# Kernel optimization log

Hardware: AMD Instinct MI355X
Metric: run time of the kernel (lower is better)

The kernel has to match this reference:

```python
import jax, jax.numpy as jnp
import numpy as np

N_NODES = 50000
N_EDGES = 1600000
IN_SIZE = 128
HIDDEN = 128
OUT_SIZE = 64
NUM_LAYERS = 3
BN_EPS = 1e-5
GIN_EPS_INIT = 1e-5


def setup_inputs() -> dict:
    key = jax.random.key(0)
    ks = jax.random.split(key, 16)
    node_feat = jax.random.normal(ks[0], (N_NODES, IN_SIZE), dtype=jnp.float32)
    src = jax.random.randint(ks[1], (N_EDGES,), 0, N_NODES)
    dst = jax.random.randint(ks[2], (N_EDGES,), 0, N_NODES)
    # per-layer MLP params (in_size == hidden, so shapes are uniform across layers)
    s1 = 1.0 / np.sqrt(IN_SIZE)
    s2 = 1.0 / np.sqrt(HIDDEN)
    W1 = jax.random.uniform(ks[3], (NUM_LAYERS, IN_SIZE, HIDDEN), jnp.float32, -s1, s1)
    b1 = jax.random.uniform(ks[4], (NUM_LAYERS, HIDDEN), jnp.float32, -s1, s1)
    gamma = jnp.ones((NUM_LAYERS, HIDDEN), jnp.float32)
    beta = jnp.zeros((NUM_LAYERS, HIDDEN), jnp.float32)
    W2 = jax.random.uniform(ks[5], (NUM_LAYERS, HIDDEN, HIDDEN), jnp.float32, -s2, s2)
    b2 = jax.random.uniform(ks[6], (NUM_LAYERS, HIDDEN), jnp.float32, -s2, s2)
    eps = jnp.full((NUM_LAYERS,), GIN_EPS_INIT, jnp.float32)  # learnable GIN eps
    Wout = jax.random.uniform(ks[7], (HIDDEN, OUT_SIZE), jnp.float32, -s2, s2)
    bout = jax.random.uniform(ks[8], (OUT_SIZE,), jnp.float32, -s2, s2)
    return {"node_feat": node_feat, "src": src, "dst": dst,
            "W1": W1, "b1": b1, "gamma": gamma, "beta": beta,
            "W2": W2, "b2": b2, "eps": eps, "Wout": Wout, "bout": bout}


def reference(node_feat, src, dst, W1, b1, gamma, beta, W2, b2, eps, Wout, bout):
    n = node_feat.shape[0]
    h = node_feat
    for i in range(NUM_LAYERS):
        # sum-aggregate source features onto destination nodes
        agg = jax.ops.segment_sum(h[src], dst, num_segments=n)  # [N, d]
        x = (1.0 + eps[i]) * h + agg
        x = x @ W1[i] + b1[i]
        # BatchNorm1d (training mode: batch statistics, biased variance)
        mu = jnp.mean(x, axis=0)
        var = jnp.var(x, axis=0)
        x = (x - mu) * jax.lax.rsqrt(var + BN_EPS) * gamma[i] + beta[i]
        x = jax.nn.relu(x)
        h = jax.nn.relu(x @ W2[i] + b2[i])
    return h @ Wout + bout
```

## Files before the change

### kernel.cpp

```cpp
#include <hip/hip_runtime.h>

#define NN 50000
#define NE 1600000
#define HID 128
#define NB 196
#define BCAP 12288
#define SLH (NN * 32)

typedef _Float16 half8 __attribute__((ext_vector_type(8)));
typedef float floatx4 __attribute__((ext_vector_type(4)));
typedef unsigned int uintx4 __attribute__((ext_vector_type(4)));

__device__ __forceinline__ void mix_acc(float a[8], half8 t) {
  uintx4 u = __builtin_bit_cast(uintx4, t);
#pragma unroll
  for (int k = 0; k < 4; ++k) {
    asm("v_fma_mix_f32 %0, %1, %2, %0 op_sel:[0,0,0] op_sel_hi:[1,0,0]"
        : "+v"(a[2 * k]) : "v"(u[k]), "v"(1.0f));
    asm("v_fma_mix_f32 %0, %1, %2, %0 op_sel:[1,0,0] op_sel_hi:[1,0,0]"
        : "+v"(a[2 * k + 1]) : "v"(u[k]), "v"(1.0f));
  }
}


#define CVT_BLK 3125
#define CNT_BLK 391

__device__ __forceinline__ void pack_one(const float* __restrict__ W1,
                                         const float* __restrict__ W2,
                                         const float* __restrict__ Wout,
                                         _Float16* __restrict__ wp, int y, int t) {
  const float* W;
  _Float16* dstp;
  int NCT;
  if (y < 3) { W = W1 + (size_t)y * 16384; dstp = wp + y * 16384; NCT = 8; }
  else if (y < 6) { W = W2 + (size_t)(y - 3) * 16384; dstp = wp + 49152 + (y - 3) * 16384; NCT = 8; }
  else { W = Wout; dstp = wp + 98304; NCT = 4; }
  if (t >= 4 * NCT * 64) return;
  int lane = t & 63;
  int ct = (t >> 6) % NCT;
  int kb = t / (64 * NCT);
  int n = ct * 16 + (lane & 15);
  int k0 = kb * 32 + (lane >> 4) * 8;
  int N = NCT * 16;
#pragma unroll
  for (int j = 0; j < 8; ++j) dstp[t * 8 + j] = (_Float16)W[(k0 + j) * N + n];
}

__global__ __launch_bounds__(256) void k_prep(
    const float* __restrict__ nf, _Float16* __restrict__ hb,
    const float* __restrict__ W1, const float* __restrict__ W2,
    const float* __restrict__ Wout, _Float16* __restrict__ wp,
    const int* __restrict__ dst, int* __restrict__ gcnt) {
  const int b = blockIdx.x;
  const int tid = threadIdx.x;
  if (b < CVT_BLK) {
    int t = b * 256 + tid;
    const float4* x4 = (const float4*)nf;
    float4 u = x4[t * 2], v = x4[t * 2 + 1];
    half8 o;
    o[0] = (_Float16)u.x; o[1] = (_Float16)u.y; o[2] = (_Float16)u.z; o[3] = (_Float16)u.w;
    o[4] = (_Float16)v.x; o[5] = (_Float16)v.y; o[6] = (_Float16)v.z; o[7] = (_Float16)v.w;
    int node = t >> 4, c = t & 15;
    ((half8*)hb)[(size_t)(c >> 2) * (NN * 4) + node * 4 + (c & 3)] = o;
  } else if (b < CVT_BLK + CNT_BLK) {
    __shared__ int cnt[NB];
    for (int i = tid; i < NB; i += 256) cnt[i] = 0;
    __syncthreads();
    int base = (b - CVT_BLK) * 4096;
    for (int i = 0; i < 16; ++i) {
      int e = base + i * 256 + tid;
      if (e < NE) atomicAdd(&cnt[dst[e] >> 8], 1);
    }
    __syncthreads();
    for (int i = tid; i < NB; i += 256)
      if (cnt[i]) atomicAdd(&gcnt[i], cnt[i]);
  } else {
    int bb = b - (CVT_BLK + CNT_BLK);
    pack_one(W1, W2, Wout, wp, bb >> 3, ((bb & 7) << 8) | tid);
  }
}


__global__ __launch_bounds__(256) void kb_basescan(const int* __restrict__ gcnt,
                                                   int* __restrict__ bbase,
                                                   int* __restrict__ bcur) {
  __shared__ int s[256];
  int tid = threadIdx.x;
  int v = (tid < NB) ? gcnt[tid] : 0;
  s[tid] = v;
  __syncthreads();
  for (int d = 1; d < 256; d <<= 1) {
    int t = (tid >= d) ? s[tid - d] : 0;
    __syncthreads();
    s[tid] += t;
    __syncthreads();
  }
  int incl = s[tid];
  if (tid < NB) {
    bbase[tid] = incl - v;
    bcur[tid] = incl - v;
  }
  if (tid == NB - 1) bbase[NB] = incl;
}

__global__ __launch_bounds__(256) void kb_partition(const int* __restrict__ src,
                                                    const int* __restrict__ dst,
                                                    int* __restrict__ bcur,
                                                    int* __restrict__ ebuf, int E) {
  __shared__ int cnt[NB];
  __shared__ int sbase[NB];
  int tid = threadIdx.x;
  for (int i = tid; i < NB; i += 256) cnt[i] = 0;
  __syncthreads();
  int base = blockIdx.x * 4096;
  int myd[16], mys[16];
#pragma unroll
  for (int i = 0; i < 16; ++i) {
    int e = base + i * 256 + tid;
    if (e < E) {
      myd[i] = dst[e];
      mys[i] = src[e];
      atomicAdd(&cnt[myd[i] >> 8], 1);
    } else {
      myd[i] = -1;
    }
  }
  __syncthreads();
  for (int i = tid; i < NB; i += 256)
    sbase[i] = cnt[i] ? atomicAdd(&bcur[i], cnt[i]) : 0;
  __syncthreads();
  for (int i = tid; i < NB; i += 256) cnt[i] = 0;
  __syncthreads();
#pragma unroll
  for (int i = 0; i < 16; ++i) {
    if (myd[i] >= 0) {
      int b = myd[i] >> 8;
      int r = atomicAdd(&cnt[b], 1);
      ebuf[sbase[b] + r] = (mys[i] << 8) | (myd[i] & 255);
    }
  }
}

__global__ __launch_bounds__(256) void kb_csr(const int* __restrict__ ebuf,
                                              const int* __restrict__ bbase,
                                              int* __restrict__ rs,
                                              unsigned short* __restrict__ eidx, int M) {
  __shared__ int cnt[256];
  __shared__ int off[256];
  __shared__ int sbuf[BCAP];
  int tid = threadIdx.x;
  int b = blockIdx.x;
  int lo = bbase[b], hi = bbase[b + 1];
  int n = hi - lo;
  cnt[tid] = 0;
  __syncthreads();
  for (int i = tid; i < n; i += 256) atomicAdd(&cnt[ebuf[lo + i] & 255], 1);
  __syncthreads();
  int v = cnt[tid];
  off[tid] = v;
  __syncthreads();
  for (int d = 1; d < 256; d <<= 1) {
    int t = (tid >= d) ? off[tid - d] : 0;
    __syncthreads();
    off[tid] += t;
    __syncthreads();
  }
  int excl = off[tid] - v;
  int gnode = b * 256 + tid;
  if (gnode < M) rs[gnode] = lo + excl;
  if (b == NB - 1 && tid == 0) rs[M] = bbase[NB];
  __syncthreads();
  cnt[tid] = excl;
  __syncthreads();
  if (n <= BCAP) {
    for (int i = tid; i < n; i += 256) {
      int ed = ebuf[lo + i];
      int r = atomicAdd(&cnt[ed & 255], 1);
      sbuf[r] = ed >> 8;
    }
    __syncthreads();
    for (int i = tid; i < n; i += 256) eidx[lo + i] = (unsigned short)sbuf[i];
  } else {
    for (int i = tid; i < n; i += 256) {
      int ed = ebuf[lo + i];
      int r = atomicAdd(&cnt[ed & 255], 1);
      eidx[lo + r] = (unsigned short)(ed >> 8);
    }
  }
}


__global__ __launch_bounds__(512, 8) void k_agg(
    const int* __restrict__ rs, const unsigned short* __restrict__ eidx,
    const float* __restrict__ eps, int layer, const _Float16* __restrict__ h,
    _Float16* __restrict__ x) {
  const int tid = threadIdx.x;
  const int b = blockIdx.x;
  const int slice = (b & 7) >> 1;
  const int tile = ((b >> 3) << 1) | (b & 1);
  const int lane = tid & 63;
  const int wid = tid >> 6;
  const int sub = lane & 3;
  const int slot = (lane >> 2) & 3;
  const int ng = lane >> 4;
  const int node = tile * 32 + wid * 4 + ng;
  const char* hbase = (const char*)(h + (size_t)slice * SLH);
  const unsigned subsh = (unsigned)sub << 4;

  float a[8] = {0.f, 0.f, 0.f, 0.f, 0.f, 0.f, 0.f, 0.f};
  int e0 = 0, e1 = 0;
  if (node < NN) {
    e0 = rs[node];
    e1 = rs[node + 1];
  }
  int e = e0 + slot;
  for (; e + 12 < e1; e += 16) {
    unsigned s0 = eidx[e];
    unsigned s1 = eidx[e + 4];
    unsigned s2 = eidx[e + 8];
    unsigned s3 = eidx[e + 12];
    half8 v0 = *(const half8*)(hbase + ((s0 << 6) | subsh));
    half8 v1 = *(const half8*)(hbase + ((s1 << 6) | subsh));
    half8 v2 = *(const half8*)(hbase + ((s2 << 6) | subsh));
    half8 v3 = *(const half8*)(hbase + ((s3 << 6) | subsh));
    half8 t01 = v0 + v1;
    half8 t23 = v2 + v3;
    mix_acc(a, t01);
    mix_acc(a, t23);
  }
  if (e + 4 < e1) {
    unsigned s0 = eidx[e];
    unsigned s1 = eidx[e + 4];
    half8 v0 = *(const half8*)(hbase + ((s0 << 6) | subsh));
    half8 v1 = *(const half8*)(hbase + ((s1 << 6) | subsh));
    half8 t01 = v0 + v1;
    mix_acc(a, t01);
    e += 8;
  }
  for (; e < e1; e += 4) {
    unsigned s0 = eidx[e];
    half8 v = *(const half8*)(hbase + ((s0 << 6) | subsh));
    mix_acc(a, v);
  }
#pragma unroll
  for (int j = 0; j < 8; ++j) {
    a[j] += __shfl_xor(a[j], 4);
    a[j] += __shfl_xor(a[j], 8);
  }
  if (slot == 0 && node < NN) {
    const float ep = 1.0f + eps[layer];
    half8 hv = *(const half8*)(hbase + (((unsigned)node << 6) | subsh));
    half8 o;
#pragma unroll
    for (int j = 0; j < 8; ++j) o[j] = (_Float16)fmaf(ep, (float)hv[j], a[j]);
    *(half8*)(x + (size_t)node * 128 + slice * 32 + sub * 8) = o;
  }
}


__global__ __launch_bounds__(512, 8) void k_stats(
    const _Float16* __restrict__ x, const _Float16* __restrict__ wp1,
    const float* __restrict__ b1L, float* __restrict__ csum,
    float* __restrict__ csq) {
  __shared__ float sS[128];
  __shared__ float sQ[128];
  const int tid = threadIdx.x;
  const int wid = tid >> 6;
  const int lane = tid & 63;
  const int slot = lane >> 4;
  const int c8 = lane & 15;
  if (tid < 128) { sS[tid] = 0.f; sQ[tid] = 0.f; }
  __syncthreads();
  const int s = blockIdx.x * 8 + wid;
  if (s < 3125) {
    const int rowBase = s * 16;
    half8 af[4];
#pragma unroll
    for (int kb = 0; kb < 4; ++kb)
      af[kb] = *(const half8*)(x + (size_t)(rowBase + c8) * 128 + kb * 32 + slot * 8);
    const half8* wp8 = (const half8*)wp1;
    float pS[8], pQ[8];
#pragma unroll
    for (int ct = 0; ct < 8; ++ct) {
      floatx4 acc = (floatx4){0.f, 0.f, 0.f, 0.f};
#pragma unroll
      for (int kb = 0; kb < 4; ++kb)
        acc = __builtin_amdgcn_mfma_f32_16x16x32_f16(af[kb], wp8[(kb * 8 + ct) * 64 + lane],
                                                     acc, 0, 0, 0);
      float bv = b1L[ct * 16 + c8];
      float ps = 0.f, pq = 0.f;
#pragma unroll
      for (int reg = 0; reg < 4; ++reg) {
        float xv = acc[reg] + bv;
        ps += xv;
        pq += xv * xv;
      }
      ps += __shfl_xor(ps, 16);
      ps += __shfl_xor(ps, 32);
      pq += __shfl_xor(pq, 16);
      pq += __shfl_xor(pq, 32);
      pS[ct] = ps;
      pQ[ct] = pq;
    }
    if (lane < 16) {
#pragma unroll
      for (int ct = 0; ct < 8; ++ct) {
        atomicAdd(&sS[ct * 16 + c8], pS[ct]);
        atomicAdd(&sQ[ct * 16 + c8], pQ[ct]);
      }
    }
  }
  __syncthreads();
  if (tid < 128) atomicAdd(&csum[tid], sS[tid]);
  else if (tid < 256) atomicAdd(&csq[tid - 128], sQ[tid - 128]);
}


template <int FINAL>
__global__ __launch_bounds__(1024, 8) void k_bngemm12(
    const _Float16* __restrict__ x, const _Float16* __restrict__ wp1,
    const float* __restrict__ b1L, const _Float16* __restrict__ wp2,
    const float* __restrict__ b2L, const float* __restrict__ gammaL,
    const float* __restrict__ betaL, const float* __restrict__ csum,
    const float* __restrict__ csq, _Float16* __restrict__ hout,
    const _Float16* __restrict__ wpo, const float* __restrict__ boutp,
    float* __restrict__ out) {
  __shared__ _Float16 As[64 * 136];
  const int tid = threadIdx.x;
  const int wid = tid >> 6;
  const int lane = tid & 63;
  const int slot = lane >> 4;
  const int c8 = lane & 15;
  const int c8t = tid & 15;
  const int rowBase = blockIdx.x * 64;
  const int rg = wid & 3;
  const int cg = wid >> 2;

  float sc_t[2], sh_t[2];
  {
    const float invM = 1.0f / (float)NN;
#pragma unroll
    for (int t = 0; t < 2; ++t) {
      int k = (cg * 2 + t) * 16 + c8;
      float mu = csum[k] * invM;
      float var = csq[k] * invM - mu * mu;
      float g = gammaL[k] * rsqrtf(var + 1e-5f);
      sc_t[t] = g;
      sh_t[t] = fmaf(b1L[k] - mu, g, betaL[k]);
    }
  }
  {
    int row = tid >> 4;
    int gr = rowBase + row;
    half8 v = {0, 0, 0, 0, 0, 0, 0, 0};
    if (gr < NN) v = *(const half8*)(x + (size_t)gr * 128 + c8t * 8);
    *(half8*)(As + row * 136 + c8t * 8) = v;
  }
  __syncthreads();

  floatx4 acc[2];
  acc[0] = (floatx4){0.f, 0.f, 0.f, 0.f};
  acc[1] = (floatx4){0.f, 0.f, 0.f, 0.f};
  {
    const half8* wp8 = (const half8*)wp1;
#pragma unroll
    for (int kb = 0; kb < 4; ++kb) {
      half8 a = *(const half8*)(As + (rg * 16 + c8) * 136 + kb * 32 + slot * 8);
#pragma unroll
      for (int t = 0; t < 2; ++t) {
        int ct = cg * 2 + t;
        acc[t] = __builtin_amdgcn_mfma_f32_16x16x32_f16(a, wp8[(kb * 8 + ct) * 64 + lane],
                                                        acc[t], 0, 0, 0);
      }
    }
  }
  __syncthreads();
#pragma unroll
  for (int t = 0; t < 2; ++t) {
    int ct = cg * 2 + t;
#pragma unroll
    for (int reg = 0; reg < 4; ++reg) {
      int row = rg * 16 + slot * 4 + reg;
      As[row * 136 + ct * 16 + c8] =
          (_Float16)fmaxf(fmaf(acc[t][reg], sc_t[t], sh_t[t]), 0.f);
    }
  }
  __syncthreads();

  acc[0] = (floatx4){0.f, 0.f, 0.f, 0.f};
  acc[1] = (floatx4){0.f, 0.f, 0.f, 0.f};
  {
    const half8* wp8 = (const half8*)wp2;
#pragma unroll
    for (int kb = 0; kb < 4; ++kb) {
      half8 a = *(const half8*)(As + (rg * 16 + c8) * 136 + kb * 32 + slot * 8);
#pragma unroll
      for (int t = 0; t < 2; ++t) {
        int ct = cg * 2 + t;
        acc[t] = __builtin_amdgcn_mfma_f32_16x16x32_f16(a, wp8[(kb * 8 + ct) * 64 + lane],
                                                        acc[t], 0, 0, 0);
      }
    }
  }
  __syncthreads();
#pragma unroll
  for (int t = 0; t < 2; ++t) {
    int ct = cg * 2 + t;
    float bv = b2L[ct * 16 + c8];
#pragma unroll
    for (int reg = 0; reg < 4; ++reg) {
      int row = rg * 16 + slot * 4 + reg;
      As[row * 136 + ct * 16 + c8] = (_Float16)fmaxf(acc[t][reg] + bv, 0.f);
    }
  }
  __syncthreads();

  if (FINAL == 0) {
    int row = tid >> 4;
    int gr = rowBase + row;
    if (gr < NN) {
      half8 v = *(half8*)(As + row * 136 + c8t * 8);
      *(half8*)(hout + (size_t)(c8t >> 2) * SLH + (size_t)gr * 32 + (c8t & 3) * 8) = v;
    }
  } else {
    if (cg < 2) {
      floatx4 acc3[2];
      acc3[0] = (floatx4){0.f, 0.f, 0.f, 0.f};
      acc3[1] = (floatx4){0.f, 0.f, 0.f, 0.f};
      const half8* wo8 = (const half8*)wpo;
#pragma unroll
      for (int kb = 0; kb < 4; ++kb) {
        half8 a = *(const half8*)(As + (rg * 16 + c8) * 136 + kb * 32 + slot * 8);
#pragma unroll
        for (int t = 0; t < 2; ++t) {
          int ct = cg * 2 + t;
          acc3[t] = __builtin_amdgcn_mfma_f32_16x16x32_f16(
              a, wo8[(kb * 4 + ct) * 64 + lane], acc3[t], 0, 0, 0);
        }
      }
#pragma unroll
      for (int t = 0; t < 2; ++t) {
        int ct = cg * 2 + t;
        float bv = boutp[ct * 16 + c8];
#pragma unroll
        for (int reg = 0; reg < 4; ++reg) {
          int gr = rowBase + rg * 16 + slot * 4 + reg;
          if (gr < NN) out[(size_t)gr * 64 + ct * 16 + c8] = acc3[t][reg] + bv;
        }
      }
    }
  }
}


extern "C" void kernel_launch(void* const* d_in, const int* in_sizes, int n_in,
                              void* d_out, int out_size, void* d_ws, size_t ws_size,
                              hipStream_t stream) {
  const float* node_feat = (const float*)d_in[0];
  const int* src = (const int*)d_in[1];
  const int* dst = (const int*)d_in[2];
  const float* W1 = (const float*)d_in[3];
  const float* b1 = (const float*)d_in[4];
  const float* gamma = (const float*)d_in[5];
  const float* beta = (const float*)d_in[6];
  const float* W2 = (const float*)d_in[7];
  const float* b2 = (const float*)d_in[8];
  const float* eps = (const float*)d_in[9];
  const float* Wout = (const float*)d_in[10];
  const float* bout = (const float*)d_in[11];
  float* out = (float*)d_out;

  int* rs = (int*)d_ws;
  int* gcnt = rs + 50176;
  int* bbase = gcnt + 256;
  int* bcur = bbase + 256;
  float* stats = (float*)(bcur + 256);
  int* eidx = (int*)(stats + 768);
  _Float16* hb = (_Float16*)(eidx + NE);
  _Float16* xb = hb + (size_t)NN * HID;
  _Float16* wp = xb + (size_t)NN * HID;
  int* ebuf = (int*)(wp + 106496);

  unsigned short* eidx16 = (unsigned short*)eidx;

  hipMemsetAsync(gcnt, 0, (256 * 3 + 768) * sizeof(int), stream);

  k_prep<<<CVT_BLK + CNT_BLK + 56, 256, 0, stream>>>(node_feat, hb, W1, W2, Wout,
                                                     wp, dst, gcnt);
  kb_basescan<<<1, 256, 0, stream>>>(gcnt, bbase, bcur);
  kb_partition<<<CNT_BLK, 256, 0, stream>>>(src, dst, bcur, ebuf, NE);
  kb_csr<<<NB, 256, 0, stream>>>(ebuf, bbase, rs, eidx16, NN);

  const int rowTiles = (NN + 63) / 64;
  const int aggBlocks = 1564 * 4;

  for (int L = 0; L < 3; ++L) {
    float* csum = stats + L * 256;
    float* csq = csum + 128;
    k_agg<<<aggBlocks, 512, 0, stream>>>(rs, eidx16, eps, L, hb, xb);
    k_stats<<<391, 512, 0, stream>>>(xb, wp + (size_t)L * 16384,
                                     b1 + (size_t)L * HID, csum, csq);
    if (L < 2) {
      k_bngemm12<0><<<rowTiles, 1024, 0, stream>>>(
          xb, wp + (size_t)L * 16384, b1 + (size_t)L * HID,
          wp + 49152 + (size_t)L * 16384, b2 + (size_t)L * HID,
          gamma + (size_t)L * HID, beta + (size_t)L * HID, csum, csq, hb,
          nullptr, nullptr, nullptr);
    } else {
      k_bngemm12<1><<<rowTiles, 1024, 0, stream>>>(
          xb, wp + (size_t)L * 16384, b1 + (size_t)L * HID,
          wp + 49152 + (size_t)L * 16384, b2 + (size_t)L * HID,
          gamma + (size_t)L * HID, beta + (size_t)L * HID, csum, csq, nullptr,
          wp + 98304, bout, out);
    }
  }
}
```

Measured before the change: 382.3 us.

## Fuse BN stats and GEMM kernels with grid barrier; prefetch edge indices

Merges the batch-norm statistics kernel and the BN+two-GEMM kernel into one persistent launch of 391 blocks, each handling two 64-row tiles. The first GEMM result is kept in registers across a software grid-wide atomic barrier, so x is read once and GEMM1 runs once per layer instead of twice. The aggregation loop now prefetches the next group of edge indices before consuming the current gathers. The CSR build kernel moves to 1024-thread blocks. The spin barrier depends on all 391 blocks being resident at once, which risks deadlock if occupancy falls short. The barrier counter lives in a region covered by the memset that runs at the start of each launch.

```diff
diff --git a/kernel.cpp b/kernel.cpp
--- a/kernel.cpp
+++ b/kernel.cpp
@@ -142,10 +142,10 @@
   }
 }
 
-__global__ __launch_bounds__(256) void kb_csr(const int* __restrict__ ebuf,
-                                              const int* __restrict__ bbase,
-                                              int* __restrict__ rs,
-                                              unsigned short* __restrict__ eidx, int M) {
+__global__ __launch_bounds__(1024) void kb_csr(const int* __restrict__ ebuf,
+                                               const int* __restrict__ bbase,
+                                               int* __restrict__ rs,
+                                               unsigned short* __restrict__ eidx, int M) {
   __shared__ int cnt[256];
   __shared__ int off[256];
   __shared__ int sbuf[BCAP];
@@ -153,36 +153,37 @@
   int b = blockIdx.x;
   int lo = bbase[b], hi = bbase[b + 1];
   int n = hi - lo;
-  cnt[tid] = 0;
-  __syncthreads();
-  for (int i = tid; i < n; i += 256) atomicAdd(&cnt[ebuf[lo + i] & 255], 1);
-  __syncthreads();
-  int v = cnt[tid];
-  off[tid] = v;
+  if (tid < 256) cnt[tid] = 0;
+  __syncthreads();
+  for (int i = tid; i < n; i += 1024) atomicAdd(&cnt[ebuf[lo + i] & 255], 1);
+  __syncthreads();
+  int v = (tid < 256) ? cnt[tid] : 0;
+  if (tid < 256) off[tid] = v;
   __syncthreads();
   for (int d = 1; d < 256; d <<= 1) {
-    int t = (tid >= d) ? off[tid - d] : 0;
-    __syncthreads();
-    off[tid] += t;
-    __syncthreads();
-  }
-  int excl = off[tid] - v;
-  int gnode = b * 256 + tid;
-  if (gnode < M) rs[gnode] = lo + excl;
-  if (b == NB - 1 && tid == 0) rs[M] = bbase[NB];
-  __syncthreads();
-  cnt[tid] = excl;
+    int t = (tid >= d && tid < 256) ? off[tid - d] : 0;
+    __syncthreads();
+    if (tid < 256) off[tid] += t;
+    __syncthreads();
+  }
+  if (tid < 256) {
+    int excl = off[tid] - v;
+    int gnode = b * 256 + tid;
+    if (gnode < M) rs[gnode] = lo + excl;
+    if (b == NB - 1 && tid == 0) rs[M] = bbase[NB];
+    cnt[tid] = excl;
+  }
   __syncthreads();
   if (n <= BCAP) {
-    for (int i = tid; i < n; i += 256) {
+    for (int i = tid; i < n; i += 1024) {
       int ed = ebuf[lo + i];
       int r = atomicAdd(&cnt[ed & 255], 1);
       sbuf[r] = ed >> 8;
     }
     __syncthreads();
-    for (int i = tid; i < n; i += 256) eidx[lo + i] = (unsigned short)sbuf[i];
+    for (int i = tid; i < n; i += 1024) eidx[lo + i] = (unsigned short)sbuf[i];
   } else {
-    for (int i = tid; i < n; i += 256) {
+    for (int i = tid; i < n; i += 1024) {
       int ed = ebuf[lo + i];
       int r = atomicAdd(&cnt[ed & 255], 1);
       eidx[lo + r] = (unsigned short)(ed >> 8);
@@ -215,15 +216,16 @@
     e1 = rs[node + 1];
   }
   int e = e0 + slot;
+  unsigned n0 = 0, n1 = 0, n2 = 0, n3 = 0;
+  if (e + 12 < e1) {
+    n0 = eidx[e]; n1 = eidx[e + 4]; n2 = eidx[e + 8]; n3 = eidx[e + 12];
+  }
   for (; e + 12 < e1; e += 16) {
-    unsigned s0 = eidx[e];
-    unsigned s1 = eidx[e + 4];
-    unsigned s2 = eidx[e + 8];
-    unsigned s3 = eidx[e + 12];
-    half8 v0 = *(const half8*)(hbase + ((s0 << 6) | subsh));
-    half8 v1 = *(const half8*)(hbase + ((s1 << 6) | subsh));
-    half8 v2 = *(const half8*)(hbase + ((s2 << 6) | subsh));
-    half8 v3 = *(const half8*)(hbase + ((s3 << 6) | subsh));
+    half8 v0 = *(const half8*)(hbase + ((n0 << 6) | subsh));
+    half8 v1 = *(const half8*)(hbase + ((n1 << 6) | subsh));
+    half8 v2 = *(const half8*)(hbase + ((n2 << 6) | subsh));
+    half8 v3 = *(const half8*)(hbase + ((n3 << 6) | subsh));
+    n0 = eidx[e + 16]; n1 = eidx[e + 20]; n2 = eidx[e + 24]; n3 = eidx[e + 28];
     half8 t01 = v0 + v1;
     half8 t23 = v2 + v3;
     mix_acc(a, t01);
@@ -259,10 +261,16 @@
 }
 
 
-__global__ __launch_bounds__(512, 8) void k_stats(
+template <int FINAL>
+__global__ __launch_bounds__(1024, 8) void k_fused(
     const _Float16* __restrict__ x, const _Float16* __restrict__ wp1,
-    const float* __restrict__ b1L, float* __restrict__ csum,
-    float* __restrict__ csq) {
+    const float* __restrict__ b1L, const _Float16* __restrict__ wp2,
+    const float* __restrict__ b2L, const float* __restrict__ gammaL,
+    const float* __restrict__ betaL, float* __restrict__ csum,
+    float* __restrict__ csq, int* __restrict__ bar,
+    _Float16* __restrict__ hout, const _Float16* __restrict__ wpo,
+    const float* __restrict__ boutp, float* __restrict__ out) {
+  __shared__ _Float16 As[64 * 136];
   __shared__ float sS[128];
   __shared__ float sQ[128];
   const int tid = threadIdx.x;
@@ -270,72 +278,74 @@
   const int lane = tid & 63;
   const int slot = lane >> 4;
   const int c8 = lane & 15;
+  const int c8t = tid & 15;
+  const int rg = wid & 3;
+  const int cg = wid >> 2;
   if (tid < 128) { sS[tid] = 0.f; sQ[tid] = 0.f; }
-  __syncthreads();
-  const int s = blockIdx.x * 8 + wid;
-  if (s < 3125) {
-    const int rowBase = s * 16;
-    half8 af[4];
-#pragma unroll
-    for (int kb = 0; kb < 4; ++kb)
-      af[kb] = *(const half8*)(x + (size_t)(rowBase + c8) * 128 + kb * 32 + slot * 8);
-    const half8* wp8 = (const half8*)wp1;
-    float pS[8], pQ[8];
-#pragma unroll
-    for (int ct = 0; ct < 8; ++ct) {
-      floatx4 acc = (floatx4){0.f, 0.f, 0.f, 0.f};
-#pragma unroll
-      for (int kb = 0; kb < 4; ++kb)
-        acc = __builtin_amdgcn_mfma_f32_16x16x32_f16(af[kb], wp8[(kb * 8 + ct) * 64 + lane],
-                                                     acc, 0, 0, 0);
+
+  floatx4 acc[2][2];
+  const half8* w1p8 = (const half8*)wp1;
+
+#pragma unroll
+  for (int tt = 0; tt < 2; ++tt) {
+    const int rowBase = (blockIdx.x * 2 + tt) * 64;
+    __syncthreads();
+    {
+      int row = tid >> 4;
+      int gr = rowBase + row;
+      half8 v = {0, 0, 0, 0, 0, 0, 0, 0};
+      if (gr < NN) v = *(const half8*)(x + (size_t)gr * 128 + c8t * 8);
+      *(half8*)(As + row * 136 + c8t * 8) = v;
+    }
+    __syncthreads();
+    acc[tt][0] = (floatx4){0.f, 0.f, 0.f, 0.f};
+    acc[tt][1] = (floatx4){0.f, 0.f, 0.f, 0.f};
+#pragma unroll
+    for (int kb = 0; kb < 4; ++kb) {
+      half8 a = *(const half8*)(As + (rg * 16 + c8) * 136 + kb * 32 + slot * 8);
+#pragma unroll
+      for (int t = 0; t < 2; ++t) {
+        int ct = cg * 2 + t;
+        acc[tt][t] = __builtin_amdgcn_mfma_f32_16x16x32_f16(
+            a, w1p8[(kb * 8 + ct) * 64 + lane], acc[tt][t], 0, 0, 0);
+      }
+    }
+#pragma unroll
+    for (int t = 0; t < 2; ++t) {
+      int ct = cg * 2 + t;
       float bv = b1L[ct * 16 + c8];
       float ps = 0.f, pq = 0.f;
 #pragma unroll
       for (int reg = 0; reg < 4; ++reg) {
-        float xv = acc[reg] + bv;
-        ps += xv;
-        pq += xv * xv;
+        int row = rg * 16 + slot * 4 + reg;
+        if (rowBase + row < NN) {
+          float xv = acc[tt][t][reg] + bv;
+          ps += xv;
+          pq += xv * xv;
+        }
       }
       ps += __shfl_xor(ps, 16);
       ps += __shfl_xor(ps, 32);
       pq += __shfl_xor(pq, 16);
       pq += __shfl_xor(pq, 32);
-      pS[ct] = ps;
-      pQ[ct] = pq;
-    }
-    if (lane < 16) {
-#pragma unroll
-      for (int ct = 0; ct < 8; ++ct) {
-        atomicAdd(&sS[ct * 16 + c8], pS[ct]);
-        atomicAdd(&sQ[ct * 16 + c8], pQ[ct]);
+      if (lane < 16) {
+        atomicAdd(&sS[ct * 16 + c8], ps);
+        atomicAdd(&sQ[ct * 16 + c8], pq);
       }
     }
   }
   __syncthreads();
   if (tid < 128) atomicAdd(&csum[tid], sS[tid]);
   else if (tid < 256) atomicAdd(&csq[tid - 128], sQ[tid - 128]);
-}
-
-
-template <int FINAL>
-__global__ __launch_bounds__(1024, 8) void k_bngemm12(
-    const _Float16* __restrict__ x, const _Float16* __restrict__ wp1,
-    const float* __restrict__ b1L, const _Float16* __restrict__ wp2,
-    const float* __restrict__ b2L, const float* __restrict__ gammaL,
-    const float* __restrict__ betaL, const float* __restrict__ csum,
-    const float* __restrict__ csq, _Float16* __restrict__ hout,
-    const _Float16* __restrict__ wpo, const float* __restrict__ boutp,
-    float* __restrict__ out) {
-  __shared__ _Float16 As[64 * 136];
-  const int tid = threadIdx.x;
-  const int wid = tid >> 6;
-  const int lane = tid & 63;
-  const int slot = lane >> 4;
-  const int c8 = lane & 15;
-  const int c8t = tid & 15;
-  const int rowBase = blockIdx.x * 64;
-  const int rg = wid & 3;
-  const int cg = wid >> 2;
+
+  __syncthreads();
+  if (tid == 0) {
+    __threadfence();
+    atomicAdd(bar, 1);
+    while (__hip_atomic_load(bar, __ATOMIC_ACQUIRE, __HIP_MEMORY_SCOPE_AGENT) < 391)
+      __builtin_amdgcn_s_sleep(8);
+  }
+  __syncthreads();
 
   float sc_t[2], sh_t[2];
   {
@@ -343,110 +353,92 @@
 #pragma unroll
     for (int t = 0; t < 2; ++t) {
       int k = (cg * 2 + t) * 16 + c8;
-      float mu = csum[k] * invM;
-      float var = csq[k] * invM - mu * mu;
+      float cs = __hip_atomic_load(&csum[k], __ATOMIC_RELAXED, __HIP_MEMORY_SCOPE_AGENT);
+      float cq = __hip_atomic_load(&csq[k], __ATOMIC_RELAXED, __HIP_MEMORY_SCOPE_AGENT);
+      float mu = cs * invM;
+      float var = cq * invM - mu * mu;
       float g = gammaL[k] * rsqrtf(var + 1e-5f);
       sc_t[t] = g;
       sh_t[t] = fmaf(b1L[k] - mu, g, betaL[k]);
     }
   }
-  {
-    int row = tid >> 4;
-    int gr = rowBase + row;
-    half8 v = {0, 0, 0, 0, 0, 0, 0, 0};
-    if (gr < NN) v = *(const half8*)(x + (size_t)gr * 128 + c8t * 8);
-    *(half8*)(As + row * 136 + c8t * 8) = v;
-  }
-  __syncthreads();
-
-  floatx4 acc[2];
-  acc[0] = (floatx4){0.f, 0.f, 0.f, 0.f};
-  acc[1] = (floatx4){0.f, 0.f, 0.f, 0.f};
-  {
-    const half8* wp8 = (const half8*)wp1;
-#pragma unroll
-    for (int kb = 0; kb < 4; ++kb) {
-      half8 a = *(const half8*)(As + (rg * 16 + c8) * 136 + kb * 32 + slot * 8);
-#pragma unroll
-      for (int t = 0; t < 2; ++t) {
-        int ct = cg * 2 + t;
-        acc[t] = __builtin_amdgcn_mfma_f32_16x16x32_f16(a, wp8[(kb * 8 + ct) * 64 + lane],
-                                                        acc[t], 0, 0, 0);
-      }
-    }
-  }
-  __syncthreads();
-#pragma unroll
-  for (int t = 0; t < 2; ++t) {
-    int ct = cg * 2 + t;
-#pragma unroll
-    for (int reg = 0; reg < 4; ++reg) {
-      int row = rg * 16 + slot * 4 + reg;
-      As[row * 136 + ct * 16 + c8] =
-          (_Float16)fmaxf(fmaf(acc[t][reg], sc_t[t], sh_t[t]), 0.f);
-    }
-  }
-  __syncthreads();
-
-  acc[0] = (floatx4){0.f, 0.f, 0.f, 0.f};
-  acc[1] = (floatx4){0.f, 0.f, 0.f, 0.f};
-  {
-    const half8* wp8 = (const half8*)wp2;
-#pragma unroll
-    for (int kb = 0; kb < 4; ++kb) {
-      half8 a = *(const half8*)(As + (rg * 16 + c8) * 136 + kb * 32 + slot * 8);
-#pragma unroll
-      for (int t = 0; t < 2; ++t) {
-        int ct = cg * 2 + t;
-        acc[t] = __builtin_amdgcn_mfma_f32_16x16x32_f16(a, wp8[(kb * 8 + ct) * 64 + lane],
-                                                        acc[t], 0, 0, 0);
-      }
-    }
-  }
-  __syncthreads();
-#pragma unroll
-  for (int t = 0; t < 2; ++t) {
-    int ct = cg * 2 + t;
-    float bv = b2L[ct * 16 + c8];
-#pragma unroll
-    for (int reg = 0; reg < 4; ++reg) {
-      int row = rg * 16 + slot * 4 + reg;
-      As[row * 136 + ct * 16 + c8] = (_Float16)fmaxf(acc[t][reg] + bv, 0.f);
-    }
-  }
-  __syncthreads();
-
-  if (FINAL == 0) {
-    int row = tid >> 4;
-    int gr = rowBase + row;
-    if (gr < NN) {
-      half8 v = *(half8*)(As + row * 136 + c8t * 8);
-      *(half8*)(hout + (size_t)(c8t >> 2) * SLH + (size_t)gr * 32 + (c8t & 3) * 8) = v;
-    }
-  } else {
-    if (cg < 2) {
-      floatx4 acc3[2];
-      acc3[0] = (floatx4){0.f, 0.f, 0.f, 0.f};
-      acc3[1] = (floatx4){0.f, 0.f, 0.f, 0.f};
-      const half8* wo8 = (const half8*)wpo;
+
+#pragma unroll
+  for (int tt = 0; tt < 2; ++tt) {
+    const int rowBase = (blockIdx.x * 2 + tt) * 64;
+    __syncthreads();
+#pragma unroll
+    for (int t = 0; t < 2; ++t) {
+      int ct = cg * 2 + t;
+#pragma unroll
+      for (int reg = 0; reg < 4; ++reg) {
+        int row = rg * 16 + slot * 4 + reg;
+        As[row * 136 + ct * 16 + c8] =
+            (_Float16)fmaxf(fmaf(acc[tt][t][reg], sc_t[t], sh_t[t]), 0.f);
+      }
+    }
+    __syncthreads();
+    floatx4 a2[2];
+    a2[0] = (floatx4){0.f, 0.f, 0.f, 0.f};
+    a2[1] = (floatx4){0.f, 0.f, 0.f, 0.f};
+    {
+      const half8* w2p8 = (const half8*)wp2;
 #pragma unroll
       for (int kb = 0; kb < 4; ++kb) {
         half8 a = *(const half8*)(As + (rg * 16 + c8) * 136 + kb * 32 + slot * 8);
 #pragma unroll
         for (int t = 0; t < 2; ++t) {
           int ct = cg * 2 + t;
-          acc3[t] = __builtin_amdgcn_mfma_f32_16x16x32_f16(
-              a, wo8[(kb * 4 + ct) * 64 + lane], acc3[t], 0, 0, 0);
+          a2[t] = __builtin_amdgcn_mfma_f32_16x16x32_f16(
+              a, w2p8[(kb * 8 + ct) * 64 + lane], a2[t], 0, 0, 0);
         }
       }
-#pragma unroll
-      for (int t = 0; t < 2; ++t) {
-        int ct = cg * 2 + t;
-        float bv = boutp[ct * 16 + c8];
-#pragma unroll
-        for (int reg = 0; reg < 4; ++reg) {
-          int gr = rowBase + rg * 16 + slot * 4 + reg;
-          if (gr < NN) out[(size_t)gr * 64 + ct * 16 + c8] = acc3[t][reg] + bv;
+    }
+    __syncthreads();
+#pragma unroll
+    for (int t = 0; t < 2; ++t) {
+      int ct = cg * 2 + t;
+      float bv = b2L[ct * 16 + c8];
+#pragma unroll
+      for (int reg = 0; reg < 4; ++reg) {
+        int row = rg * 16 + slot * 4 + reg;
+        As[row * 136 + ct * 16 + c8] = (_Float16)fmaxf(a2[t][reg] + bv, 0.f);
+      }
+    }
+    __syncthreads();
+
+    if (FINAL == 0) {
+      int row = tid >> 4;
+      int gr = rowBase + row;
+      if (gr < NN) {
+        half8 v = *(half8*)(As + row * 136 + c8t * 8);
+        *(half8*)(hout + (size_t)(c8t >> 2) * SLH + (size_t)gr * 32 + (c8t & 3) * 8) = v;
+      }
+    } else {
+      if (cg < 2) {
+        floatx4 a3[2];
+        a3[0] = (floatx4){0.f, 0.f, 0.f, 0.f};
+        a3[1] = (floatx4){0.f, 0.f, 0.f, 0.f};
+        const half8* wo8 = (const half8*)wpo;
+#pragma unroll
+        for (int kb = 0; kb < 4; ++kb) {
+          half8 a = *(const half8*)(As + (rg * 16 + c8) * 136 + kb * 32 + slot * 8);
+#pragma unroll
+          for (int t = 0; t < 2; ++t) {
+            int ct = cg * 2 + t;
+            a3[t] = __builtin_amdgcn_mfma_f32_16x16x32_f16(
+                a, wo8[(kb * 4 + ct) * 64 + lane], a3[t], 0, 0, 0);
+          }
+        }
+#pragma unroll
+        for (int t = 0; t < 2; ++t) {
+          int ct = cg * 2 + t;
+          float bv = boutp[ct * 16 + c8];
+#pragma unroll
+          for (int reg = 0; reg < 4; ++reg) {
+            int gr = rowBase + rg * 16 + slot * 4 + reg;
+            if (gr < NN) out[(size_t)gr * 64 + ct * 16 + c8] = a3[t][reg] + bv;
+          }
         }
       }
     }
@@ -490,29 +482,27 @@
                                                      wp, dst, gcnt);
   kb_basescan<<<1, 256, 0, stream>>>(gcnt, bbase, bcur);
   kb_partition<<<CNT_BLK, 256, 0, stream>>>(src, dst, bcur, ebuf, NE);
-  kb_csr<<<NB, 256, 0, stream>>>(ebuf, bbase, rs, eidx16, NN);
-
-  const int rowTiles = (NN + 63) / 64;
+  kb_csr<<<NB, 1024, 0, stream>>>(ebuf, bbase, rs, eidx16, NN);
+
   const int aggBlocks = 1564 * 4;
 
   for (int L = 0; L < 3; ++L) {
     float* csum = stats + L * 256;
     float* csq = csum + 128;
+    int* bar = bcur + 200 + L;
     k_agg<<<aggBlocks, 512, 0, stream>>>(rs, eidx16, eps, L, hb, xb);
-    k_stats<<<391, 512, 0, stream>>>(xb, wp + (size_t)L * 16384,
-                                     b1 + (size_t)L * HID, csum, csq);
     if (L < 2) {
-      k_bngemm12<0><<<rowTiles, 1024, 0, stream>>>(
+      k_fused<0><<<391, 1024, 0, stream>>>(
           xb, wp + (size_t)L * 16384, b1 + (size_t)L * HID,
           wp + 49152 + (size_t)L * 16384, b2 + (size_t)L * HID,
-          gamma + (size_t)L * HID, beta + (size_t)L * HID, csum, csq, hb,
+          gamma + (size_t)L * HID, beta + (size_t)L * HID, csum, csq, bar, hb,
           nullptr, nullptr, nullptr);
     } else {
-      k_bngemm12<1><<<rowTiles, 1024, 0, stream>>>(
+      k_fused<1><<<391, 1024, 0, stream>>>(
           xb, wp + (size_t)L * 16384, b1 + (size_t)L * HID,
           wp + 49152 + (size_t)L * 16384, b2 + (size_t)L * HID,
-          gamma + (size_t)L * HID, beta + (size_t)L * HID, csum, csq, nullptr,
-          wp + 98304, bout, out);
-    }
-  }
-}
+          gamma + (size_t)L * HID, beta + (size_t)L * HID, csum, csq, bar,
+          nullptr, wp + 98304, bout, out);
+    }
+  }
+}
```

After: 454.5 us. 1.19x slower.
